# Optimization experiments

Hardware: AMD Instinct MI355X
Metric: run time of the kernel (lower is better)

The kernel has to match this reference:

```python
import jax, jax.numpy as jnp
import numpy as np

B = 1024        # number of graphs
MAXLEN = 64     # max nodes per graph (pad_sequence length)
E = 256         # hidden_size
H = 8           # num_heads
HD = E // H     # head dim
NEG = -1e9


def setup_inputs() -> dict:
    key = jax.random.key(0)
    k0, k1, k2 = jax.random.split(key, 3)
    lens = np.tile(np.array([32, 48, 64, 40], dtype=np.int64), B // 4)  # sum = 47104
    batch_indices = jnp.asarray(np.repeat(np.arange(B, dtype=np.int64), lens))
    N = int(lens.sum())
    node_features = jax.random.normal(k0, (N, E), dtype=jnp.float32)
    in_proj_w = jax.random.normal(k1, (3 * E, E), dtype=jnp.float32) * (1.0 / np.sqrt(E))
    in_proj_b = jnp.zeros((3 * E,), dtype=jnp.float32)
    out_proj_w = jax.random.normal(k2, (E, E), dtype=jnp.float32) * (1.0 / np.sqrt(E))
    out_proj_b = jnp.zeros((E,), dtype=jnp.float32)
    return {"node_features": node_features, "batch_indices": batch_indices,
            "in_proj_w": in_proj_w, "in_proj_b": in_proj_b,
            "out_proj_w": out_proj_w, "out_proj_b": out_proj_b}


def _pad_ragged(node_features, batch_indices):
    # counts per graph, start offset of each graph, position of each node in its graph
    N = node_features.shape[0]
    counts = jax.ops.segment_sum(jnp.ones((N,), jnp.int32), batch_indices, num_segments=B)
    starts = jnp.cumsum(counts) - counts
    pos = jnp.arange(N) - starts[batch_indices]
    padded = jnp.zeros((B, MAXLEN, E), node_features.dtype).at[batch_indices, pos].set(node_features)
    key_pad = jnp.arange(MAXLEN)[None, :] >= counts[:, None]  # [B, L] True = padding
    return padded, key_pad


def reference(node_features, batch_indices, in_proj_w, in_proj_b, out_proj_w, out_proj_b):
    padded, key_pad = _pad_ragged(node_features, batch_indices)   # [B,L,E], [B,L]
    qkv = padded @ in_proj_w.T + in_proj_b                        # [B,L,3E]
    q, k, v = jnp.split(qkv, 3, axis=-1)
    q = q.reshape(B, MAXLEN, H, HD)
    k = k.reshape(B, MAXLEN, H, HD)
    v = v.reshape(B, MAXLEN, H, HD)
    scores = jnp.einsum('blhd,bmhd->bhlm', q, k) / jnp.sqrt(jnp.float32(HD))
    scores = jnp.where(key_pad[:, None, None, :], NEG, scores)    # mask padded keys
    attn = jax.nn.softmax(scores, axis=-1)                        # [B,H,L,L]
    ctx = jnp.einsum('bhlm,bmhd->blhd', attn, v).reshape(B, MAXLEN, E)
    out = ctx @ out_proj_w.T + out_proj_b                         # [B,L,E]
    out = jnp.transpose(out, (1, 0, 2))                           # [L,B,E] seq-first like torch
    weights = attn.mean(axis=1)                                   # [B,L,L] head-averaged
    return out, weights
```

## Files before the change

### kernel.cpp

```cpp
#include <hip/hip_runtime.h>

typedef unsigned short u16;
typedef short bf16x8 __attribute__((ext_vector_type(8)));
typedef float f32x4 __attribute__((ext_vector_type(4)));

#define MFMA16(a, b, c) __builtin_amdgcn_mfma_f32_16x16x32_bf16((a), (b), (c), 0, 0, 0)

static __device__ __forceinline__ u16 f2bf(float f) {
    union { float f; unsigned int u; } v; v.f = f;
    unsigned int u = v.u;
    u += 0x7fffu + ((u >> 16) & 1u);
    return (u16)(u >> 16);
}

__global__ void prep_kernel(const int* __restrict__ bidx, int N,
                            const float* __restrict__ w_in, const float* __restrict__ w_out,
                            int* __restrict__ starts, int* __restrict__ counts,
                            u16* __restrict__ w_in_bf, u16* __restrict__ w_out_bf) {
    int tid = blockIdx.x * blockDim.x + threadIdx.x;
    if (tid < 1024) {
        int lo = 0, hi = N;
        while (lo < hi) { int mid = (lo + hi) >> 1; if (bidx[mid] < tid) lo = mid + 1; else hi = mid; }
        int s0 = lo;
        lo = 0; hi = N;
        int v1 = tid + 1;
        while (lo < hi) { int mid = (lo + hi) >> 1; if (bidx[mid] < v1) lo = mid + 1; else hi = mid; }
        starts[tid] = s0;
        counts[tid] = lo - s0;
    }
    if (tid < 49152) {
        float4 v = ((const float4*)w_in)[tid];
        ushort4 o; o.x = f2bf(v.x); o.y = f2bf(v.y); o.z = f2bf(v.z); o.w = f2bf(v.w);
        ((ushort4*)w_in_bf)[tid] = o;
    }
    if (tid < 16384) {
        float4 v = ((const float4*)w_out)[tid];
        ushort4 o; o.x = f2bf(v.x); o.y = f2bf(v.y); o.z = f2bf(v.z); o.w = f2bf(v.w);
        ((ushort4*)w_out_bf)[tid] = o;
    }
}

__global__ __launch_bounds__(256, 1) void gat_kernel(
    const float* __restrict__ X, const float* __restrict__ bias_in,
    const float* __restrict__ bias_out,
    const int* __restrict__ starts, const int* __restrict__ counts,
    const u16* __restrict__ w_in_bf, const u16* __restrict__ w_out_bf,
    float* __restrict__ out, float* __restrict__ wout) {

    __shared__ u16 x_s[64][264];
    __shared__ u16 q_s[64][264];
    __shared__ u16 k_s[64][264];
    __shared__ u16 v_t[256][72];
    __shared__ u16 p_s[4][16][72];

    const int b = blockIdx.x;
    const int tid = threadIdx.x;
    const int w = tid >> 6;
    const int lane = tid & 63;
    const int n = lane & 15;
    const int quad = lane >> 4;
    const int s = starts[b];
    const int c = counts[b];

    #pragma unroll
    for (int i = 0; i < 16; ++i) {
        int f4 = i * 256 + tid;
        int row = f4 >> 6, c4 = f4 & 63;
        float4 v = make_float4(0.f, 0.f, 0.f, 0.f);
        if (row < c) v = ((const float4*)X)[(s + row) * 64 + c4];
        ushort4 o; o.x = f2bf(v.x); o.y = f2bf(v.y); o.z = f2bf(v.z); o.w = f2bf(v.w);
        *(ushort4*)&x_s[row][c4 * 4] = o;
    }
    __syncthreads();

    bf16x8 afr[4][8];
    #pragma unroll
    for (int st = 0; st < 4; ++st)
        #pragma unroll
        for (int ks = 0; ks < 8; ++ks)
            afr[st][ks] = *(const bf16x8*)&x_s[st * 16 + n][ks * 32 + quad * 8];

    #pragma unroll 1
    for (int ct = w; ct < 48; ct += 4) {
        bf16x8 bfr[8];
        const u16* wr = w_in_bf + (ct * 16 + n) * 256 + quad * 8;
        #pragma unroll
        for (int ks = 0; ks < 8; ++ks) bfr[ks] = *(const bf16x8*)(wr + ks * 32);
        float bias = bias_in[ct * 16 + n];

        f32x4 acc[4];
        #pragma unroll
        for (int st = 0; st < 4; ++st) acc[st] = (f32x4){0.f, 0.f, 0.f, 0.f};
        #pragma unroll
        for (int ks = 0; ks < 8; ++ks)
            #pragma unroll
            for (int st = 0; st < 4; ++st)
                acc[st] = MFMA16(afr[st][ks], bfr[ks], acc[st]);

        #pragma unroll
        for (int st = 0; st < 4; ++st) {
            if (ct < 32) {
                u16 (*dst)[264] = (ct < 16) ? q_s : k_s;
                int cc = (ct * 16 + n) & 255;
                #pragma unroll
                for (int r = 0; r < 4; ++r)
                    dst[st * 16 + quad * 4 + r][cc] = f2bf(acc[st][r] + bias);
            } else {
                int vcol = (ct - 32) * 16 + n;
                ushort4 pk;
                pk.x = f2bf(acc[st][0] + bias); pk.y = f2bf(acc[st][1] + bias);
                pk.z = f2bf(acc[st][2] + bias); pk.w = f2bf(acc[st][3] + bias);
                *(ushort4*)&v_t[vcol][st * 16 + quad * 4] = pk;
            }
        }
    }
    __syncthreads();

    const float scale = 0.17677669529663687f;
    const int m0 = w * 16;
    float wacc[4][4];
    #pragma unroll
    for (int t = 0; t < 4; ++t)
        #pragma unroll
        for (int r = 0; r < 4; ++r) wacc[t][r] = 0.f;
    f32x4 ctx[8][2];
    #pragma unroll
    for (int h = 0; h < 8; ++h) { ctx[h][0] = (f32x4){0,0,0,0}; ctx[h][1] = (f32x4){0,0,0,0}; }

    #pragma unroll 1
    for (int h = 0; h < 8; ++h) {
        bf16x8 aq = *(const bf16x8*)&q_s[m0 + n][h * 32 + quad * 8];
        f32x4 sc[4];
        #pragma unroll
        for (int t = 0; t < 4; ++t) {
            bf16x8 bk = *(const bf16x8*)&k_s[t * 16 + n][h * 32 + quad * 8];
            f32x4 z = (f32x4){0.f, 0.f, 0.f, 0.f};
            sc[t] = MFMA16(aq, bk, z);
        }
        float p[4][4], inv[4];
        #pragma unroll
        for (int r = 0; r < 4; ++r) {
            float mx = -1e30f;
            #pragma unroll
            for (int t = 0; t < 4; ++t) {
                float sv = ((t * 16 + n) < c) ? sc[t][r] * scale : -1e30f;
                p[t][r] = sv;
                mx = fmaxf(mx, sv);
            }
            #pragma unroll
            for (int d = 1; d < 16; d <<= 1) mx = fmaxf(mx, __shfl_xor(mx, d, 64));
            float sm = 0.f;
            #pragma unroll
            for (int t = 0; t < 4; ++t) {
                float e = ((t * 16 + n) < c) ? __expf(p[t][r] - mx) : 0.f;
                p[t][r] = e; sm += e;
            }
            #pragma unroll
            for (int d = 1; d < 16; d <<= 1) sm += __shfl_xor(sm, d, 64);
            inv[r] = 1.f / sm;
            #pragma unroll
            for (int t = 0; t < 4; ++t) wacc[t][r] += p[t][r] * (inv[r] * 0.125f);
        }
        #pragma unroll
        for (int t = 0; t < 4; ++t)
            #pragma unroll
            for (int r = 0; r < 4; ++r)
                p_s[w][quad * 4 + r][t * 16 + n] = f2bf(p[t][r]);
        #pragma unroll
        for (int nt = 0; nt < 2; ++nt) {
            f32x4 acc = (f32x4){0.f, 0.f, 0.f, 0.f};
            #pragma unroll
            for (int k2 = 0; k2 < 2; ++k2) {
                bf16x8 ap = *(const bf16x8*)&p_s[w][n][k2 * 32 + quad * 8];
                bf16x8 bv = *(const bf16x8*)&v_t[h * 32 + nt * 16 + n][k2 * 32 + quad * 8];
                acc = MFMA16(ap, bv, acc);
            }
            #pragma unroll
            for (int r = 0; r < 4; ++r) ctx[h][nt][r] = acc[r] * inv[r];
        }
    }

    #pragma unroll
    for (int t = 0; t < 4; ++t)
        #pragma unroll
        for (int r = 0; r < 4; ++r)
            wout[b * 4096 + (m0 + quad * 4 + r) * 64 + t * 16 + n] = wacc[t][r];

    #pragma unroll
    for (int h = 0; h < 8; ++h)
        #pragma unroll
        for (int nt = 0; nt < 2; ++nt)
            #pragma unroll
            for (int r = 0; r < 4; ++r)
                x_s[m0 + quad * 4 + r][h * 32 + nt * 16 + n] = f2bf(ctx[h][nt][r]);

    bf16x8 actx[8];
    #pragma unroll
    for (int ks = 0; ks < 8; ++ks)
        actx[ks] = *(const bf16x8*)&x_s[m0 + n][ks * 32 + quad * 8];

    #pragma unroll 2
    for (int ct = 0; ct < 16; ++ct) {
        bf16x8 bfr[8];
        const u16* wr = w_out_bf + (ct * 16 + n) * 256 + quad * 8;
        #pragma unroll
        for (int ks = 0; ks < 8; ++ks) bfr[ks] = *(const bf16x8*)(wr + ks * 32);
        f32x4 acc = (f32x4){0.f, 0.f, 0.f, 0.f};
        #pragma unroll
        for (int ks = 0; ks < 8; ++ks) acc = MFMA16(actx[ks], bfr[ks], acc);
        float bias = bias_out[ct * 16 + n];
        #pragma unroll
        for (int r = 0; r < 4; ++r)
            out[(m0 + quad * 4 + r) * 262144 + b * 256 + ct * 16 + n] = acc[r] + bias;
    }
}

extern "C" void kernel_launch(void* const* d_in, const int* in_sizes, int n_in,
                              void* d_out, int out_size, void* d_ws, size_t ws_size,
                              hipStream_t stream) {
    const float* X     = (const float*)d_in[0];
    const int*   bidx  = (const int*)d_in[1];
    const float* w_in  = (const float*)d_in[2];
    const float* b_in  = (const float*)d_in[3];
    const float* w_out = (const float*)d_in[4];
    const float* b_out = (const float*)d_in[5];
    const int N = in_sizes[1];

    float* out  = (float*)d_out;
    float* wout = out + 64 * 1024 * 256;

    int* starts   = (int*)d_ws;
    int* counts   = starts + 1024;
    u16* w_in_bf  = (u16*)(counts + 1024);
    u16* w_out_bf = w_in_bf + 196608;

    hipLaunchKernelGGL(prep_kernel, dim3(256), dim3(256), 0, stream,
                       bidx, N, w_in, w_out, starts, counts, w_in_bf, w_out_bf);
    hipLaunchKernelGGL(gat_kernel, dim3(1024), dim3(256), 0, stream,
                       X, b_in, b_out, starts, counts, w_in_bf, w_out_bf, out, wout);
}
```

Before: 321.1 us.

## Process heads in groups to shrink LDS and allow two blocks per CU

Splits the fused QKV projection into four head-pair groups, computing Q/K/V for two heads at a time into small shared buffers and running attention on them before moving on. X is loaded straight from global into MFMA registers instead of being staged through shared memory, and the context is written directly to a shared buffer rather than held in registers. Shared-memory use drops substantially and launch bounds are raised to two blocks per CU to improve occupancy. The cost is extra barriers per group, and the higher occupancy target puts pressure on registers, which may cause spills given the large afr fragment array.

New measurement: 282.9 us. 11.9% less time.

```diff
diff --git a/kernel.cpp b/kernel.cpp
--- a/kernel.cpp
+++ b/kernel.cpp
@@ -28,7 +28,7 @@
         starts[tid] = s0;
         counts[tid] = lo - s0;
     }
-    if (tid < 49152) {
+    {
         float4 v = ((const float4*)w_in)[tid];
         ushort4 o; o.x = f2bf(v.x); o.y = f2bf(v.y); o.z = f2bf(v.z); o.w = f2bf(v.w);
         ((ushort4*)w_in_bf)[tid] = o;
@@ -40,18 +40,18 @@
     }
 }
 
-__global__ __launch_bounds__(256, 1) void gat_kernel(
+__global__ __launch_bounds__(256, 2) void gat_kernel(
     const float* __restrict__ X, const float* __restrict__ bias_in,
     const float* __restrict__ bias_out,
     const int* __restrict__ starts, const int* __restrict__ counts,
     const u16* __restrict__ w_in_bf, const u16* __restrict__ w_out_bf,
     float* __restrict__ out, float* __restrict__ wout) {
 
-    __shared__ u16 x_s[64][264];
-    __shared__ u16 q_s[64][264];
-    __shared__ u16 k_s[64][264];
-    __shared__ u16 v_t[256][72];
+    __shared__ u16 qg[64][72];
+    __shared__ u16 kg[64][72];
+    __shared__ u16 vt[64][72];
     __shared__ u16 p_s[4][16][72];
+    __shared__ u16 cs[64][264];
 
     const int b = blockIdx.x;
     const int tid = threadIdx.x;
@@ -61,123 +61,133 @@
     const int quad = lane >> 4;
     const int s = starts[b];
     const int c = counts[b];
-
-    #pragma unroll
-    for (int i = 0; i < 16; ++i) {
-        int f4 = i * 256 + tid;
-        int row = f4 >> 6, c4 = f4 & 63;
-        float4 v = make_float4(0.f, 0.f, 0.f, 0.f);
-        if (row < c) v = ((const float4*)X)[(s + row) * 64 + c4];
-        ushort4 o; o.x = f2bf(v.x); o.y = f2bf(v.y); o.z = f2bf(v.z); o.w = f2bf(v.w);
-        *(ushort4*)&x_s[row][c4 * 4] = o;
-    }
-    __syncthreads();
+    const int m0 = w * 16;
 
     bf16x8 afr[4][8];
     #pragma unroll
-    for (int st = 0; st < 4; ++st)
-        #pragma unroll
-        for (int ks = 0; ks < 8; ++ks)
-            afr[st][ks] = *(const bf16x8*)&x_s[st * 16 + n][ks * 32 + quad * 8];
+    for (int st = 0; st < 4; ++st) {
+        int row = st * 16 + n;
+        bool ok = row < c;
+        const float* src = X + (long)(s + row) * 256 + quad * 8;
+        #pragma unroll
+        for (int ks = 0; ks < 8; ++ks) {
+            float4 v0 = make_float4(0.f, 0.f, 0.f, 0.f);
+            float4 v1 = make_float4(0.f, 0.f, 0.f, 0.f);
+            if (ok) {
+                v0 = *(const float4*)(src + ks * 32);
+                v1 = *(const float4*)(src + ks * 32 + 4);
+            }
+            bf16x8 a;
+            a[0] = (short)f2bf(v0.x); a[1] = (short)f2bf(v0.y);
+            a[2] = (short)f2bf(v0.z); a[3] = (short)f2bf(v0.w);
+            a[4] = (short)f2bf(v1.x); a[5] = (short)f2bf(v1.y);
+            a[6] = (short)f2bf(v1.z); a[7] = (short)f2bf(v1.w);
+            afr[st][ks] = a;
+        }
+    }
+
+    const float scale = 0.17677669529663687f;
+    float wacc[4][4];
+    #pragma unroll
+    for (int t = 0; t < 4; ++t)
+        #pragma unroll
+        for (int r = 0; r < 4; ++r) wacc[t][r] = 0.f;
 
     #pragma unroll 1
-    for (int ct = w; ct < 48; ct += 4) {
-        bf16x8 bfr[8];
-        const u16* wr = w_in_bf + (ct * 16 + n) * 256 + quad * 8;
-        #pragma unroll
-        for (int ks = 0; ks < 8; ++ks) bfr[ks] = *(const bf16x8*)(wr + ks * 32);
-        float bias = bias_in[ct * 16 + n];
-
-        f32x4 acc[4];
-        #pragma unroll
-        for (int st = 0; st < 4; ++st) acc[st] = (f32x4){0.f, 0.f, 0.f, 0.f};
-        #pragma unroll
-        for (int ks = 0; ks < 8; ++ks)
-            #pragma unroll
-            for (int st = 0; st < 4; ++st)
-                acc[st] = MFMA16(afr[st][ks], bfr[ks], acc[st]);
-
-        #pragma unroll
-        for (int st = 0; st < 4; ++st) {
-            if (ct < 32) {
-                u16 (*dst)[264] = (ct < 16) ? q_s : k_s;
-                int cc = (ct * 16 + n) & 255;
+    for (int g = 0; g < 4; ++g) {
+        #pragma unroll 1
+        for (int i = 0; i < 3; ++i) {
+            int j = w + i * 4;
+            int type = j >> 2;
+            int sub = j & 3;
+            int wrow = type * 256 + g * 64 + sub * 16 + n;
+            bf16x8 bfr[8];
+            const u16* wr = w_in_bf + wrow * 256 + quad * 8;
+            #pragma unroll
+            for (int ks = 0; ks < 8; ++ks) bfr[ks] = *(const bf16x8*)(wr + ks * 32);
+            float bias = bias_in[wrow];
+
+            f32x4 acc[4];
+            #pragma unroll
+            for (int st = 0; st < 4; ++st) acc[st] = (f32x4){0.f, 0.f, 0.f, 0.f};
+            #pragma unroll
+            for (int ks = 0; ks < 8; ++ks)
+                #pragma unroll
+                for (int st = 0; st < 4; ++st)
+                    acc[st] = MFMA16(afr[st][ks], bfr[ks], acc[st]);
+
+            #pragma unroll
+            for (int st = 0; st < 4; ++st) {
+                if (type == 2) {
+                    ushort4 pk;
+                    pk.x = f2bf(acc[st][0] + bias); pk.y = f2bf(acc[st][1] + bias);
+                    pk.z = f2bf(acc[st][2] + bias); pk.w = f2bf(acc[st][3] + bias);
+                    *(ushort4*)&vt[sub * 16 + n][st * 16 + quad * 4] = pk;
+                } else {
+                    u16 (*dst)[72] = type ? kg : qg;
+                    #pragma unroll
+                    for (int r = 0; r < 4; ++r)
+                        dst[st * 16 + quad * 4 + r][sub * 16 + n] = f2bf(acc[st][r] + bias);
+                }
+            }
+        }
+        __syncthreads();
+
+        #pragma unroll 1
+        for (int hh = 0; hh < 2; ++hh) {
+            int h = g * 2 + hh;
+            bf16x8 aq = *(const bf16x8*)&qg[m0 + n][hh * 32 + quad * 8];
+            f32x4 sc[4];
+            #pragma unroll
+            for (int t = 0; t < 4; ++t) {
+                bf16x8 bk = *(const bf16x8*)&kg[t * 16 + n][hh * 32 + quad * 8];
+                f32x4 z = (f32x4){0.f, 0.f, 0.f, 0.f};
+                sc[t] = MFMA16(aq, bk, z);
+            }
+            float p[4][4], inv[4];
+            #pragma unroll
+            for (int r = 0; r < 4; ++r) {
+                float mx = -1e30f;
+                #pragma unroll
+                for (int t = 0; t < 4; ++t) {
+                    float sv = ((t * 16 + n) < c) ? sc[t][r] * scale : -1e30f;
+                    p[t][r] = sv;
+                    mx = fmaxf(mx, sv);
+                }
+                #pragma unroll
+                for (int d = 1; d < 16; d <<= 1) mx = fmaxf(mx, __shfl_xor(mx, d, 64));
+                float sm = 0.f;
+                #pragma unroll
+                for (int t = 0; t < 4; ++t) {
+                    float e = ((t * 16 + n) < c) ? __expf(p[t][r] - mx) : 0.f;
+                    p[t][r] = e; sm += e;
+                }
+                #pragma unroll
+                for (int d = 1; d < 16; d <<= 1) sm += __shfl_xor(sm, d, 64);
+                inv[r] = 1.f / sm;
+                #pragma unroll
+                for (int t = 0; t < 4; ++t) wacc[t][r] += p[t][r] * (inv[r] * 0.125f);
+            }
+            #pragma unroll
+            for (int t = 0; t < 4; ++t)
                 #pragma unroll
                 for (int r = 0; r < 4; ++r)
-                    dst[st * 16 + quad * 4 + r][cc] = f2bf(acc[st][r] + bias);
-            } else {
-                int vcol = (ct - 32) * 16 + n;
-                ushort4 pk;
-                pk.x = f2bf(acc[st][0] + bias); pk.y = f2bf(acc[st][1] + bias);
-                pk.z = f2bf(acc[st][2] + bias); pk.w = f2bf(acc[st][3] + bias);
-                *(ushort4*)&v_t[vcol][st * 16 + quad * 4] = pk;
+                    p_s[w][quad * 4 + r][t * 16 + n] = f2bf(p[t][r]);
+            #pragma unroll
+            for (int nt = 0; nt < 2; ++nt) {
+                f32x4 acc = (f32x4){0.f, 0.f, 0.f, 0.f};
+                #pragma unroll
+                for (int k2 = 0; k2 < 2; ++k2) {
+                    bf16x8 ap = *(const bf16x8*)&p_s[w][n][k2 * 32 + quad * 8];
+                    bf16x8 bv = *(const bf16x8*)&vt[hh * 32 + nt * 16 + n][k2 * 32 + quad * 8];
+                    acc = MFMA16(ap, bv, acc);
+                }
+                #pragma unroll
+                for (int r = 0; r < 4; ++r)
+                    cs[m0 + quad * 4 + r][h * 32 + nt * 16 + n] = f2bf(acc[r] * inv[r]);
             }
         }
-    }
-    __syncthreads();
-
-    const float scale = 0.17677669529663687f;
-    const int m0 = w * 16;
-    float wacc[4][4];
-    #pragma unroll
-    for (int t = 0; t < 4; ++t)
-        #pragma unroll
-        for (int r = 0; r < 4; ++r) wacc[t][r] = 0.f;
-    f32x4 ctx[8][2];
-    #pragma unroll
-    for (int h = 0; h < 8; ++h) { ctx[h][0] = (f32x4){0,0,0,0}; ctx[h][1] = (f32x4){0,0,0,0}; }
-
-    #pragma unroll 1
-    for (int h = 0; h < 8; ++h) {
-        bf16x8 aq = *(const bf16x8*)&q_s[m0 + n][h * 32 + quad * 8];
-        f32x4 sc[4];
-        #pragma unroll
-        for (int t = 0; t < 4; ++t) {
-            bf16x8 bk = *(const bf16x8*)&k_s[t * 16 + n][h * 32 + quad * 8];
-            f32x4 z = (f32x4){0.f, 0.f, 0.f, 0.f};
-            sc[t] = MFMA16(aq, bk, z);
-        }
-        float p[4][4], inv[4];
-        #pragma unroll
-        for (int r = 0; r < 4; ++r) {
-            float mx = -1e30f;
-            #pragma unroll
-            for (int t = 0; t < 4; ++t) {
-                float sv = ((t * 16 + n) < c) ? sc[t][r] * scale : -1e30f;
-                p[t][r] = sv;
-                mx = fmaxf(mx, sv);
-            }
-            #pragma unroll
-            for (int d = 1; d < 16; d <<= 1) mx = fmaxf(mx, __shfl_xor(mx, d, 64));
-            float sm = 0.f;
-            #pragma unroll
-            for (int t = 0; t < 4; ++t) {
-                float e = ((t * 16 + n) < c) ? __expf(p[t][r] - mx) : 0.f;
-                p[t][r] = e; sm += e;
-            }
-            #pragma unroll
-            for (int d = 1; d < 16; d <<= 1) sm += __shfl_xor(sm, d, 64);
-            inv[r] = 1.f / sm;
-            #pragma unroll
-            for (int t = 0; t < 4; ++t) wacc[t][r] += p[t][r] * (inv[r] * 0.125f);
-        }
-        #pragma unroll
-        for (int t = 0; t < 4; ++t)
-            #pragma unroll
-            for (int r = 0; r < 4; ++r)
-                p_s[w][quad * 4 + r][t * 16 + n] = f2bf(p[t][r]);
-        #pragma unroll
-        for (int nt = 0; nt < 2; ++nt) {
-            f32x4 acc = (f32x4){0.f, 0.f, 0.f, 0.f};
-            #pragma unroll
-            for (int k2 = 0; k2 < 2; ++k2) {
-                bf16x8 ap = *(const bf16x8*)&p_s[w][n][k2 * 32 + quad * 8];
-                bf16x8 bv = *(const bf16x8*)&v_t[h * 32 + nt * 16 + n][k2 * 32 + quad * 8];
-                acc = MFMA16(ap, bv, acc);
-            }
-            #pragma unroll
-            for (int r = 0; r < 4; ++r) ctx[h][nt][r] = acc[r] * inv[r];
-        }
+        __syncthreads();
     }
 
     #pragma unroll
@@ -186,18 +196,10 @@
         for (int r = 0; r < 4; ++r)
             wout[b * 4096 + (m0 + quad * 4 + r) * 64 + t * 16 + n] = wacc[t][r];
 
-    #pragma unroll
-    for (int h = 0; h < 8; ++h)
-        #pragma unroll
-        for (int nt = 0; nt < 2; ++nt)
-            #pragma unroll
-            for (int r = 0; r < 4; ++r)
-                x_s[m0 + quad * 4 + r][h * 32 + nt * 16 + n] = f2bf(ctx[h][nt][r]);
-
     bf16x8 actx[8];
     #pragma unroll
     for (int ks = 0; ks < 8; ++ks)
-        actx[ks] = *(const bf16x8*)&x_s[m0 + n][ks * 32 + quad * 8];
+        actx[ks] = *(const bf16x8*)&cs[m0 + n][ks * 32 + quad * 8];
 
     #pragma unroll 2
     for (int ct = 0; ct < 16; ++ct) {
@@ -234,7 +236,7 @@
     u16* w_in_bf  = (u16*)(counts + 1024);
     u16* w_out_bf = w_in_bf + 196608;
 
-    hipLaunchKernelGGL(prep_kernel, dim3(256), dim3(256), 0, stream,
+    hipLaunchKernelGGL(prep_kernel, dim3(192), dim3(256), 0, stream,
                        bidx, N, w_in, w_out, starts, counts, w_in_bf, w_out_bf);
     hipLaunchKernelGGL(gat_kernel, dim3(1024), dim3(256), 0, stream,
                        X, b_in, b_out, starts, counts, w_in_bf, w_out_bf, out, wout);
```
